# Kernel optimization log

Measured on AMD Instinct MI355X. Metric: run time of the kernel, lower is better.

Reference implementation:

```python
import jax, jax.numpy as jnp
import numpy as np

B, F, S, D = 256, 8, 200, 64
H = 36  # hidden units per field
EPS = 1e-3  # Dice BN epsilon


def setup_inputs() -> dict:
    key0 = jax.random.key(0)
    ks = jax.random.split(key0, 8)
    query = jax.random.normal(ks[0], (B, F, D), dtype=jnp.float32)
    key = jax.random.normal(ks[1], (B, F, S, D), dtype=jnp.float32)
    sequence_num = jax.random.randint(ks[2], (B, F), 1, S + 1, dtype=jnp.int32)
    W_h = jax.random.normal(ks[3], (F, 3 * D, H), dtype=jnp.float32) * 0.05
    b_h = jnp.zeros((F, H), dtype=jnp.float32)
    alpha = jnp.zeros((F,), dtype=jnp.float32)
    W_o = jax.random.normal(ks[4], (F, H, 1), dtype=jnp.float32) * 0.05
    b_o = jnp.zeros((F, 1), dtype=jnp.float32)
    return {"query": query, "key": key, "W_h": W_h, "b_h": b_h,
            "alpha": alpha, "W_o": W_o, "b_o": b_o,
            "sequence_num": sequence_num, "training": 1}


def reference(query, key, W_h, b_h, alpha, W_o, b_o, sequence_num, training):
    # query: [B,F,D], key: [B,F,S,D]
    q = query[:, :, None, :]                      # broadcast instead of tile
    qb = jnp.broadcast_to(q, key.shape)           # [B,F,S,D]
    cat = jnp.concatenate([key, qb, q - key], axis=-1)  # [B,F,S,3D]
    # per-field Dense(36), vectorized across fields
    h = jnp.einsum('bfsc,fch->bfsh', cat, W_h) + b_h[None, :, None, :]
    # Dice: BatchNorm (no affine, training-mode batch stats over batch+seq per field/feature)
    mean = h.mean(axis=(0, 2), keepdims=True)
    var = h.var(axis=(0, 2), keepdims=True)
    p = jax.nn.sigmoid((h - mean) * jax.lax.rsqrt(var + EPS))
    h = (alpha[None, :, None, None] * (1.0 - p) + p) * h
    # per-field Dense(1) -> attention scores [B,F,S]
    scores = jnp.einsum('bfsh,fh->bfs', h, W_o[:, :, 0]) + b_o[None, :, 0, None]
    # mask invalid positions and softmax over sequence
    mask = jnp.arange(key.shape[2])[None, None, :] < sequence_num[:, :, None]
    scores = jnp.where(mask, scores, -jnp.inf)
    attn = jax.nn.softmax(scores, axis=-1)        # [B,F,S]
    # weighted sum over sequence -> [B,F,D]
    return jnp.einsum('bfs,bfsd->bfd', attn, key)
```

## Files before the change

kernel.cpp:

```cpp
#include <hip/hip_runtime.h>
#include <math.h>

#define NB 256
#define NF 8
#define NS 200
#define ND 64
#define NH 36
#define MT 13
#define EPSV 1e-3f

#define WS_SUM 0
#define WS_SQ  288
#define WS_QT  1152
#define WS_WK  (1152 + 2048 * 48)

typedef __attribute__((ext_vector_type(8))) short short8;
typedef __attribute__((ext_vector_type(4))) float f32x4;

__device__ __forceinline__ unsigned short f32_to_bf16(float x) {
    unsigned u = __float_as_uint(x);
    unsigned r = u + 0x7FFFu + ((u >> 16) & 1u);
    return (unsigned short)(r >> 16);
}
__device__ __forceinline__ float bf16_to_f32(unsigned short h) {
    return __uint_as_float(((unsigned)h) << 16);
}
__device__ __forceinline__ short8 cvt8(float4 a, float4 b) {
    short8 r;
    r[0] = (short)f32_to_bf16(a.x); r[1] = (short)f32_to_bf16(a.y);
    r[2] = (short)f32_to_bf16(a.z); r[3] = (short)f32_to_bf16(a.w);
    r[4] = (short)f32_to_bf16(b.x); r[5] = (short)f32_to_bf16(b.y);
    r[6] = (short)f32_to_bf16(b.z); r[7] = (short)f32_to_bf16(b.w);
    return r;
}

__global__ __launch_bounds__(256) void k_prep(
    const float* __restrict__ query, const float* __restrict__ W_h,
    const float* __restrict__ b_h, float* __restrict__ ws)
{
    const int blk = blockIdx.x, tid = threadIdx.x;
    if (blk < NB) {
        __shared__ float qs[NF * ND];
        for (int i = tid; i < NF * ND; i += 256)
            qs[i] = query[(size_t)blk * NF * ND + i];
        __syncthreads();
        for (int i = tid; i < NF * 48; i += 256) {
            int f = i / 48, h = i - f * 48;
            float acc = 0.f;
            if (h < NH) {
                const float* Wf = W_h + (size_t)f * (3 * ND * NH);
                acc = b_h[f * NH + h];
                for (int d = 0; d < ND; ++d)
                    acc += qs[f * ND + d] * (Wf[(ND + d) * NH + h] + Wf[(2 * ND + d) * NH + h]);
            }
            ws[WS_QT + (size_t)(blk * NF + f) * 48 + h] = acc;
        }
    } else {
        const int f = blk - NB;
        const float* Wf = W_h + (size_t)f * (3 * ND * NH);
        unsigned short* wk = (unsigned short*)(ws + WS_WK) + f * (48 * ND);
        for (int i = tid; i < 48 * ND; i += 256) {
            int h = i >> 6, d = i & 63;
            float v = (h < NH) ? (Wf[d * NH + h] - Wf[(2 * ND + d) * NH + h]) : 0.f;
            wk[h * ND + d] = f32_to_bf16(v);
        }
    }
}

__global__ __launch_bounds__(256, 4) void k_stats(
    const float* __restrict__ key, float* __restrict__ ws)
{
    const int blk = blockIdx.x;
    const int f = blk & (NF - 1);
    const int tid = threadIdx.x;
    const int lane = tid & 63;
    const int wv = tid >> 6;
    const int col = lane & 15;
    const int quad = lane >> 4;

    __shared__ float sumP[48], sqP[48];
    if (tid < 48) { sumP[tid] = 0.f; sqP[tid] = 0.f; }
    __syncthreads();

    const float* kbase = key + (size_t)blk * (NS * ND);
    const unsigned short* wk = (const unsigned short*)(ws + WS_WK) + f * (48 * ND);

    short8 bfr[3][2];
    float qv[3];
    #pragma unroll
    for (int nt = 0; nt < 3; ++nt) {
        #pragma unroll
        for (int ks = 0; ks < 2; ++ks)
            bfr[nt][ks] = *(const short8*)&wk[(nt * 16 + col) * ND + ks * 32 + quad * 8];
        qv[nt] = ws[WS_QT + (size_t)blk * 48 + nt * 16 + col];
    }

    float s_sum[3] = {0.f, 0.f, 0.f}, s_sq[3] = {0.f, 0.f, 0.f};
    for (int mt = wv; mt < MT; mt += 4) {
        const int s = 16 * mt + col;
        const float4* p = (const float4*)(kbase + (size_t)(s < NS ? s : NS - 1) * ND + quad * 8);
        float4 a0 = p[0], a1 = p[1];
        float4 b0 = p[8], b1 = p[9];
        short8 ah0 = cvt8(a0, a1);
        short8 ah1 = cvt8(b0, b1);
        #pragma unroll
        for (int nt = 0; nt < 3; ++nt) {
            f32x4 acc = {qv[nt], qv[nt], qv[nt], qv[nt]};
            acc = __builtin_amdgcn_mfma_f32_16x16x32_bf16(ah0, bfr[nt][0], acc, 0, 0, 0);
            acc = __builtin_amdgcn_mfma_f32_16x16x32_bf16(ah1, bfr[nt][1], acc, 0, 0, 0);
            #pragma unroll
            for (int r = 0; r < 4; ++r) {
                int srow = 16 * mt + quad * 4 + r;
                if (srow < NS) { float v = acc[r]; s_sum[nt] += v; s_sq[nt] += v * v; }
            }
        }
    }
    #pragma unroll
    for (int nt = 0; nt < 3; ++nt) {
        float sv = s_sum[nt], qq = s_sq[nt];
        sv += __shfl_xor(sv, 16, 64); sv += __shfl_xor(sv, 32, 64);
        qq += __shfl_xor(qq, 16, 64); qq += __shfl_xor(qq, 32, 64);
        if (quad == 0) {
            atomicAdd(&sumP[nt * 16 + col], sv);
            atomicAdd(&sqP[nt * 16 + col], qq);
        }
    }
    __syncthreads();
    if (tid < NH) {
        atomicAdd(&ws[WS_SUM + f * NH + tid], sumP[tid]);
        atomicAdd(&ws[WS_SQ + f * NH + tid], sqP[tid]);
    }
}

__global__ __launch_bounds__(256, 3) void k_attn(
    const float* __restrict__ key, const float* __restrict__ alpha,
    const float* __restrict__ W_o, const float* __restrict__ b_o,
    const int* __restrict__ seqn, const float* __restrict__ ws,
    float* __restrict__ out)
{
    const int blk = blockIdx.x;
    const int f = blk & (NF - 1);
    const int tid = threadIdx.x;
    const int lane = tid & 63;
    const int wv = tid >> 6;
    const int col = lane & 15;
    const int quad = lane >> 4;

    __shared__ float sw[208];
    __shared__ float redM[4], redS[4];
    __shared__ float pout[4][64];

    const float* kbase = key + (size_t)blk * (NS * ND);
    const unsigned short* wk = (const unsigned short*)(ws + WS_WK) + f * (48 * ND);
    const float inv_n = 1.f / (float)(NB * NS);

    short8 bfr[3][2];
    float qv[3], mn[3], iv[3], wo[3];
    #pragma unroll
    for (int nt = 0; nt < 3; ++nt) {
        #pragma unroll
        for (int ks = 0; ks < 2; ++ks)
            bfr[nt][ks] = *(const short8*)&wk[(nt * 16 + col) * ND + ks * 32 + quad * 8];
        const int hh = nt * 16 + col;
        const bool hv = hh < NH;
        const int hc = hv ? hh : 0;
        qv[nt] = ws[WS_QT + (size_t)blk * 48 + hh];
        const float sm = ws[WS_SUM + f * NH + hc];
        const float sq = ws[WS_SQ + f * NH + hc];
        const float m = sm * inv_n;
        mn[nt] = m;
        iv[nt] = rsqrtf(fmaxf(sq * inv_n - m * m, 0.f) + EPSV);
        wo[nt] = hv ? W_o[f * NH + hh] : 0.f;
    }
    const float alf = alpha[f];
    const float bo = b_o[f];
    const int sq_n = seqn[blk];

    short8 kah[4][2];
    #pragma unroll
    for (int t = 0; t < 4; ++t) {
        const int mt = wv + 4 * t;
        if (mt < MT) {
            const int s = 16 * mt + col;
            const float4* p = (const float4*)(kbase + (size_t)(s < NS ? s : NS - 1) * ND + quad * 8);
            float4 a0 = p[0], a1 = p[1];
            float4 b0 = p[8], b1 = p[9];
            kah[t][0] = cvt8(a0, a1);
            kah[t][1] = cvt8(b0, b1);
            float part[4] = {0.f, 0.f, 0.f, 0.f};
            #pragma unroll
            for (int nt = 0; nt < 3; ++nt) {
                f32x4 acc = {qv[nt], qv[nt], qv[nt], qv[nt]};
                acc = __builtin_amdgcn_mfma_f32_16x16x32_bf16(kah[t][0], bfr[nt][0], acc, 0, 0, 0);
                acc = __builtin_amdgcn_mfma_f32_16x16x32_bf16(kah[t][1], bfr[nt][1], acc, 0, 0, 0);
                #pragma unroll
                for (int r = 0; r < 4; ++r) {
                    const float h = acc[r];
                    const float pg = 1.f / (1.f + __expf(-(h - mn[nt]) * iv[nt]));
                    part[r] += (alf + (1.f - alf) * pg) * h * wo[nt];
                }
            }
            #pragma unroll
            for (int r = 0; r < 4; ++r) {
                float v = part[r];
                v += __shfl_xor(v, 1, 64);
                v += __shfl_xor(v, 2, 64);
                v += __shfl_xor(v, 4, 64);
                v += __shfl_xor(v, 8, 64);
                const int srow = 16 * mt + quad * 4 + r;
                if (col == 0 && srow < NS) sw[srow] = v + bo;
            }
        }
    }
    __syncthreads();

    const bool valid = (tid < 208) && (tid < sq_n);
    const float sc = valid ? sw[tid] : -1e30f;
    float m = sc;
    m = fmaxf(m, __shfl_xor(m, 1, 64));  m = fmaxf(m, __shfl_xor(m, 2, 64));
    m = fmaxf(m, __shfl_xor(m, 4, 64));  m = fmaxf(m, __shfl_xor(m, 8, 64));
    m = fmaxf(m, __shfl_xor(m, 16, 64)); m = fmaxf(m, __shfl_xor(m, 32, 64));
    if (lane == 0) redM[wv] = m;
    __syncthreads();
    const float maxv = fmaxf(fmaxf(redM[0], redM[1]), fmaxf(redM[2], redM[3]));
    const float e = valid ? __expf(sc - maxv) : 0.f;
    float l = e;
    l += __shfl_xor(l, 1, 64);  l += __shfl_xor(l, 2, 64);
    l += __shfl_xor(l, 4, 64);  l += __shfl_xor(l, 8, 64);
    l += __shfl_xor(l, 16, 64); l += __shfl_xor(l, 32, 64);
    if (lane == 0) redS[wv] = l;
    __syncthreads();
    const float isum = 1.f / (redS[0] + redS[1] + redS[2] + redS[3]);
    if (tid < 208) sw[tid] = e * isum;
    __syncthreads();

    float po0[8] = {0,0,0,0,0,0,0,0}, po1[8] = {0,0,0,0,0,0,0,0};
    #pragma unroll
    for (int t = 0; t < 4; ++t) {
        const int mt = wv + 4 * t;
        if (mt < MT) {
            const float w = sw[16 * mt + col];
            #pragma unroll
            for (int j = 0; j < 8; ++j) {
                po0[j] += w * bf16_to_f32((unsigned short)kah[t][0][j]);
                po1[j] += w * bf16_to_f32((unsigned short)kah[t][1][j]);
            }
        }
    }
    #pragma unroll
    for (int off = 1; off <= 8; off <<= 1) {
        #pragma unroll
        for (int j = 0; j < 8; ++j) {
            po0[j] += __shfl_xor(po0[j], off, 64);
            po1[j] += __shfl_xor(po1[j], off, 64);
        }
    }
    if (col == 0) {
        #pragma unroll
        for (int j = 0; j < 8; ++j) {
            pout[wv][quad * 8 + j] = po0[j];
            pout[wv][32 + quad * 8 + j] = po1[j];
        }
    }
    __syncthreads();
    if (tid < 64)
        out[(size_t)blk * ND + tid] =
            pout[0][tid] + pout[1][tid] + pout[2][tid] + pout[3][tid];
}

extern "C" void kernel_launch(void* const* d_in, const int* in_sizes, int n_in,
                              void* d_out, int out_size, void* d_ws, size_t ws_size,
                              hipStream_t stream) {
    const float* query = (const float*)d_in[0];
    const float* key   = (const float*)d_in[1];
    const float* W_h   = (const float*)d_in[2];
    const float* b_h   = (const float*)d_in[3];
    const float* alpha = (const float*)d_in[4];
    const float* W_o   = (const float*)d_in[5];
    const float* b_o   = (const float*)d_in[6];
    const int*   seqn  = (const int*)d_in[7];
    float* out = (float*)d_out;
    float* ws  = (float*)d_ws;

    hipMemsetAsync(ws, 0, 576 * sizeof(float), stream);
    k_prep<<<NB + NF, 256, 0, stream>>>(query, W_h, b_h, ws);
    k_stats<<<NB * NF, 256, 0, stream>>>(key, ws);
    k_attn<<<NB * NF, 256, 0, stream>>>(key, alpha, W_o, b_o, seqn, ws, out);
}
```

Measured before the change: 213.1 us.

## Process two batch rows per block, fold query term into stats algebraically

Each stats and attention block now handles two (batch, field) pairs, so half as many blocks are launched. The stats kernel no longer adds the per-row query term inside the MFMA. It adds that term afterwards in closed form, using the sums and squared sums of the key projection. The 200-row tail is peeled into a separate partial tile so the per-row bound checks go away, and the attention kernel's occupancy hint rises from 3 to 4. Float-to-bf16 conversion now truncates with a byte permute instead of rounding to nearest even, which is cheaper but slightly less accurate.

```diff
diff --git a/kernel.cpp b/kernel.cpp
--- a/kernel.cpp
+++ b/kernel.cpp
@@ -6,7 +6,6 @@
 #define NS 200
 #define ND 64
 #define NH 36
-#define MT 13
 #define EPSV 1e-3f
 
 #define WS_SUM 0
@@ -16,8 +15,9 @@
 
 typedef __attribute__((ext_vector_type(8))) short short8;
 typedef __attribute__((ext_vector_type(4))) float f32x4;
-
-__device__ __forceinline__ unsigned short f32_to_bf16(float x) {
+typedef __attribute__((ext_vector_type(4))) int int4v;
+
+__device__ __forceinline__ unsigned short f32_to_bf16_rne(float x) {
     unsigned u = __float_as_uint(x);
     unsigned r = u + 0x7FFFu + ((u >> 16) & 1u);
     return (unsigned short)(r >> 16);
@@ -25,13 +25,13 @@
 __device__ __forceinline__ float bf16_to_f32(unsigned short h) {
     return __uint_as_float(((unsigned)h) << 16);
 }
-__device__ __forceinline__ short8 cvt8(float4 a, float4 b) {
-    short8 r;
-    r[0] = (short)f32_to_bf16(a.x); r[1] = (short)f32_to_bf16(a.y);
-    r[2] = (short)f32_to_bf16(a.z); r[3] = (short)f32_to_bf16(a.w);
-    r[4] = (short)f32_to_bf16(b.x); r[5] = (short)f32_to_bf16(b.y);
-    r[6] = (short)f32_to_bf16(b.z); r[7] = (short)f32_to_bf16(b.w);
-    return r;
+__device__ __forceinline__ short8 pack8(float4 a, float4 b) {
+    int4v t;
+    t[0] = (int)__builtin_amdgcn_perm(__float_as_uint(a.y), __float_as_uint(a.x), 0x07060302u);
+    t[1] = (int)__builtin_amdgcn_perm(__float_as_uint(a.w), __float_as_uint(a.z), 0x07060302u);
+    t[2] = (int)__builtin_amdgcn_perm(__float_as_uint(b.y), __float_as_uint(b.x), 0x07060302u);
+    t[3] = (int)__builtin_amdgcn_perm(__float_as_uint(b.w), __float_as_uint(b.z), 0x07060302u);
+    return __builtin_bit_cast(short8, t);
 }
 
 __global__ __launch_bounds__(256) void k_prep(
@@ -62,7 +62,7 @@
         for (int i = tid; i < 48 * ND; i += 256) {
             int h = i >> 6, d = i & 63;
             float v = (h < NH) ? (Wf[d * NH + h] - Wf[(2 * ND + d) * NH + h]) : 0.f;
-            wk[h * ND + d] = f32_to_bf16(v);
+            wk[h * ND + d] = f32_to_bf16_rne(v);
         }
     }
 }
@@ -72,67 +72,95 @@
 {
     const int blk = blockIdx.x;
     const int f = blk & (NF - 1);
+    const int b0 = (blk >> 3) * 2;
     const int tid = threadIdx.x;
     const int lane = tid & 63;
     const int wv = tid >> 6;
     const int col = lane & 15;
     const int quad = lane >> 4;
 
-    __shared__ float sumP[48], sqP[48];
-    if (tid < 48) { sumP[tid] = 0.f; sqP[tid] = 0.f; }
+    __shared__ float sumP[2][48], sqP[2][48];
+    if (tid < 96) { int p = tid / 48, h = tid - 48 * p; sumP[p][h] = 0.f; sqP[p][h] = 0.f; }
     __syncthreads();
 
-    const float* kbase = key + (size_t)blk * (NS * ND);
     const unsigned short* wk = (const unsigned short*)(ws + WS_WK) + f * (48 * ND);
+    const float* kb0 = key + (size_t)(b0 * NF + f) * (NS * ND);
+    const float* kb1 = kb0 + (size_t)NF * NS * ND;
 
     short8 bfr[3][2];
-    float qv[3];
     #pragma unroll
-    for (int nt = 0; nt < 3; ++nt) {
+    for (int nt = 0; nt < 3; ++nt)
         #pragma unroll
         for (int ks = 0; ks < 2; ++ks)
             bfr[nt][ks] = *(const short8*)&wk[(nt * 16 + col) * ND + ks * 32 + quad * 8];
-        qv[nt] = ws[WS_QT + (size_t)blk * 48 + nt * 16 + col];
-    }
-
-    float s_sum[3] = {0.f, 0.f, 0.f}, s_sq[3] = {0.f, 0.f, 0.f};
-    for (int mt = wv; mt < MT; mt += 4) {
-        const int s = 16 * mt + col;
-        const float4* p = (const float4*)(kbase + (size_t)(s < NS ? s : NS - 1) * ND + quad * 8);
-        float4 a0 = p[0], a1 = p[1];
-        float4 b0 = p[8], b1 = p[9];
-        short8 ah0 = cvt8(a0, a1);
-        short8 ah1 = cvt8(b0, b1);
+
+    float s1[2][3] = {{0.f,0.f,0.f},{0.f,0.f,0.f}};
+    float s2[2][3] = {{0.f,0.f,0.f},{0.f,0.f,0.f}};
+
+    #pragma unroll
+    for (int i = 0; i < 3; ++i) {
+        const int s = 16 * (wv + 4 * i) + col;
+        const size_t off = (size_t)s * ND + quad * 8;
+        #pragma unroll
+        for (int p = 0; p < 2; ++p) {
+            const float4* ptr = (const float4*)((p ? kb1 : kb0) + off);
+            float4 a0 = ptr[0], a1 = ptr[1], c0 = ptr[8], c1 = ptr[9];
+            short8 fa = pack8(a0, a1);
+            short8 fb = pack8(c0, c1);
+            #pragma unroll
+            for (int nt = 0; nt < 3; ++nt) {
+                f32x4 acc = {0.f, 0.f, 0.f, 0.f};
+                acc = __builtin_amdgcn_mfma_f32_16x16x32_bf16(fa, bfr[nt][0], acc, 0, 0, 0);
+                acc = __builtin_amdgcn_mfma_f32_16x16x32_bf16(fb, bfr[nt][1], acc, 0, 0, 0);
+                #pragma unroll
+                for (int r = 0; r < 4; ++r) { float v = acc[r]; s1[p][nt] += v; s2[p][nt] += v * v; }
+            }
+        }
+    }
+    if (wv == 0) {
+        const int s = 192 + col;
+        #pragma unroll
+        for (int p = 0; p < 2; ++p) {
+            short8 fa = {0,0,0,0,0,0,0,0}, fb = {0,0,0,0,0,0,0,0};
+            if (col < 8) {
+                const float4* ptr = (const float4*)((p ? kb1 : kb0) + (size_t)s * ND + quad * 8);
+                float4 a0 = ptr[0], a1 = ptr[1], c0 = ptr[8], c1 = ptr[9];
+                fa = pack8(a0, a1); fb = pack8(c0, c1);
+            }
+            #pragma unroll
+            for (int nt = 0; nt < 3; ++nt) {
+                f32x4 acc = {0.f, 0.f, 0.f, 0.f};
+                acc = __builtin_amdgcn_mfma_f32_16x16x32_bf16(fa, bfr[nt][0], acc, 0, 0, 0);
+                acc = __builtin_amdgcn_mfma_f32_16x16x32_bf16(fb, bfr[nt][1], acc, 0, 0, 0);
+                #pragma unroll
+                for (int r = 0; r < 4; ++r) { float v = acc[r]; s1[p][nt] += v; s2[p][nt] += v * v; }
+            }
+        }
+    }
+    #pragma unroll
+    for (int p = 0; p < 2; ++p)
         #pragma unroll
         for (int nt = 0; nt < 3; ++nt) {
-            f32x4 acc = {qv[nt], qv[nt], qv[nt], qv[nt]};
-            acc = __builtin_amdgcn_mfma_f32_16x16x32_bf16(ah0, bfr[nt][0], acc, 0, 0, 0);
-            acc = __builtin_amdgcn_mfma_f32_16x16x32_bf16(ah1, bfr[nt][1], acc, 0, 0, 0);
-            #pragma unroll
-            for (int r = 0; r < 4; ++r) {
-                int srow = 16 * mt + quad * 4 + r;
-                if (srow < NS) { float v = acc[r]; s_sum[nt] += v; s_sq[nt] += v * v; }
-            }
-        }
-    }
-    #pragma unroll
-    for (int nt = 0; nt < 3; ++nt) {
-        float sv = s_sum[nt], qq = s_sq[nt];
-        sv += __shfl_xor(sv, 16, 64); sv += __shfl_xor(sv, 32, 64);
-        qq += __shfl_xor(qq, 16, 64); qq += __shfl_xor(qq, 32, 64);
-        if (quad == 0) {
-            atomicAdd(&sumP[nt * 16 + col], sv);
-            atomicAdd(&sqP[nt * 16 + col], qq);
-        }
-    }
+            float a = s1[p][nt], c = s2[p][nt];
+            a += __shfl_xor(a, 16, 64); a += __shfl_xor(a, 32, 64);
+            c += __shfl_xor(c, 16, 64); c += __shfl_xor(c, 32, 64);
+            if (quad == 0) {
+                atomicAdd(&sumP[p][nt * 16 + col], a);
+                atomicAdd(&sqP[p][nt * 16 + col], c);
+            }
+        }
     __syncthreads();
-    if (tid < NH) {
-        atomicAdd(&ws[WS_SUM + f * NH + tid], sumP[tid]);
-        atomicAdd(&ws[WS_SQ + f * NH + tid], sqP[tid]);
-    }
-}
-
-__global__ __launch_bounds__(256, 3) void k_attn(
+    if (tid < 72) {
+        const int p = (tid >= NH) ? 1 : 0;
+        const int h = tid - NH * p;
+        const float S1 = sumP[p][h], S2 = sqP[p][h];
+        const float qt = ws[WS_QT + (size_t)((b0 + p) * NF + f) * 48 + h];
+        atomicAdd(&ws[WS_SUM + f * NH + h], S1 + 200.f * qt);
+        atomicAdd(&ws[WS_SQ  + f * NH + h], S2 + 2.f * qt * S1 + 200.f * qt * qt);
+    }
+}
+
+__global__ __launch_bounds__(256, 4) void k_attn(
     const float* __restrict__ key, const float* __restrict__ alpha,
     const float* __restrict__ W_o, const float* __restrict__ b_o,
     const int* __restrict__ seqn, const float* __restrict__ ws,
@@ -140,6 +168,7 @@
 {
     const int blk = blockIdx.x;
     const int f = blk & (NF - 1);
+    const int b0 = (blk >> 3) * 2;
     const int tid = threadIdx.x;
     const int lane = tid & 63;
     const int wv = tid >> 6;
@@ -150,12 +179,11 @@
     __shared__ float redM[4], redS[4];
     __shared__ float pout[4][64];
 
-    const float* kbase = key + (size_t)blk * (NS * ND);
     const unsigned short* wk = (const unsigned short*)(ws + WS_WK) + f * (48 * ND);
     const float inv_n = 1.f / (float)(NB * NS);
 
     short8 bfr[3][2];
-    float qv[3], mn[3], iv[3], wo[3];
+    float mn[3], iv[3], wo[3];
     #pragma unroll
     for (int nt = 0; nt < 3; ++nt) {
         #pragma unroll
@@ -164,7 +192,6 @@
         const int hh = nt * 16 + col;
         const bool hv = hh < NH;
         const int hc = hv ? hh : 0;
-        qv[nt] = ws[WS_QT + (size_t)blk * 48 + hh];
         const float sm = ws[WS_SUM + f * NH + hc];
         const float sq = ws[WS_SQ + f * NH + hc];
         const float m = sm * inv_n;
@@ -174,25 +201,31 @@
     }
     const float alf = alpha[f];
     const float bo = b_o[f];
-    const int sq_n = seqn[blk];
-
-    short8 kah[4][2];
-    #pragma unroll
-    for (int t = 0; t < 4; ++t) {
-        const int mt = wv + 4 * t;
-        if (mt < MT) {
+
+    for (int p = 0; p < 2; ++p) {
+        const int bf = (b0 + p) * NF + f;
+        const float* kbase = key + (size_t)bf * (NS * ND);
+        float qv[3];
+        #pragma unroll
+        for (int nt = 0; nt < 3; ++nt)
+            qv[nt] = ws[WS_QT + (size_t)bf * 48 + nt * 16 + col];
+        const int sq_n = seqn[bf];
+
+        short8 kah[4][2];
+        #pragma unroll
+        for (int i = 0; i < 3; ++i) {
+            const int mt = wv + 4 * i;
             const int s = 16 * mt + col;
-            const float4* p = (const float4*)(kbase + (size_t)(s < NS ? s : NS - 1) * ND + quad * 8);
-            float4 a0 = p[0], a1 = p[1];
-            float4 b0 = p[8], b1 = p[9];
-            kah[t][0] = cvt8(a0, a1);
-            kah[t][1] = cvt8(b0, b1);
+            const float4* ptr = (const float4*)(kbase + (size_t)s * ND + quad * 8);
+            float4 a0 = ptr[0], a1 = ptr[1], c0 = ptr[8], c1 = ptr[9];
+            kah[i][0] = pack8(a0, a1);
+            kah[i][1] = pack8(c0, c1);
             float part[4] = {0.f, 0.f, 0.f, 0.f};
             #pragma unroll
             for (int nt = 0; nt < 3; ++nt) {
                 f32x4 acc = {qv[nt], qv[nt], qv[nt], qv[nt]};
-                acc = __builtin_amdgcn_mfma_f32_16x16x32_bf16(kah[t][0], bfr[nt][0], acc, 0, 0, 0);
-                acc = __builtin_amdgcn_mfma_f32_16x16x32_bf16(kah[t][1], bfr[nt][1], acc, 0, 0, 0);
+                acc = __builtin_amdgcn_mfma_f32_16x16x32_bf16(kah[i][0], bfr[nt][0], acc, 0, 0, 0);
+                acc = __builtin_amdgcn_mfma_f32_16x16x32_bf16(kah[i][1], bfr[nt][1], acc, 0, 0, 0);
                 #pragma unroll
                 for (int r = 0; r < 4; ++r) {
                     const float h = acc[r];
@@ -203,69 +236,102 @@
             #pragma unroll
             for (int r = 0; r < 4; ++r) {
                 float v = part[r];
-                v += __shfl_xor(v, 1, 64);
-                v += __shfl_xor(v, 2, 64);
-                v += __shfl_xor(v, 4, 64);
-                v += __shfl_xor(v, 8, 64);
-                const int srow = 16 * mt + quad * 4 + r;
+                v += __shfl_xor(v, 1, 64); v += __shfl_xor(v, 2, 64);
+                v += __shfl_xor(v, 4, 64); v += __shfl_xor(v, 8, 64);
+                if (col == 0) sw[16 * mt + quad * 4 + r] = v + bo;
+            }
+        }
+        if (wv == 0) {
+            kah[3][0] = (short8){0,0,0,0,0,0,0,0};
+            kah[3][1] = (short8){0,0,0,0,0,0,0,0};
+            if (col < 8) {
+                const float4* ptr = (const float4*)(kbase + (size_t)(192 + col) * ND + quad * 8);
+                float4 a0 = ptr[0], a1 = ptr[1], c0 = ptr[8], c1 = ptr[9];
+                kah[3][0] = pack8(a0, a1);
+                kah[3][1] = pack8(c0, c1);
+            }
+            float part[4] = {0.f, 0.f, 0.f, 0.f};
+            #pragma unroll
+            for (int nt = 0; nt < 3; ++nt) {
+                f32x4 acc = {qv[nt], qv[nt], qv[nt], qv[nt]};
+                acc = __builtin_amdgcn_mfma_f32_16x16x32_bf16(kah[3][0], bfr[nt][0], acc, 0, 0, 0);
+                acc = __builtin_amdgcn_mfma_f32_16x16x32_bf16(kah[3][1], bfr[nt][1], acc, 0, 0, 0);
+                #pragma unroll
+                for (int r = 0; r < 4; ++r) {
+                    const float h = acc[r];
+                    const float pg = 1.f / (1.f + __expf(-(h - mn[nt]) * iv[nt]));
+                    part[r] += (alf + (1.f - alf) * pg) * h * wo[nt];
+                }
+            }
+            #pragma unroll
+            for (int r = 0; r < 4; ++r) {
+                float v = part[r];
+                v += __shfl_xor(v, 1, 64); v += __shfl_xor(v, 2, 64);
+                v += __shfl_xor(v, 4, 64); v += __shfl_xor(v, 8, 64);
+                const int srow = 192 + quad * 4 + r;
                 if (col == 0 && srow < NS) sw[srow] = v + bo;
             }
         }
-    }
-    __syncthreads();
-
-    const bool valid = (tid < 208) && (tid < sq_n);
-    const float sc = valid ? sw[tid] : -1e30f;
-    float m = sc;
-    m = fmaxf(m, __shfl_xor(m, 1, 64));  m = fmaxf(m, __shfl_xor(m, 2, 64));
-    m = fmaxf(m, __shfl_xor(m, 4, 64));  m = fmaxf(m, __shfl_xor(m, 8, 64));
-    m = fmaxf(m, __shfl_xor(m, 16, 64)); m = fmaxf(m, __shfl_xor(m, 32, 64));
-    if (lane == 0) redM[wv] = m;
-    __syncthreads();
-    const float maxv = fmaxf(fmaxf(redM[0], redM[1]), fmaxf(redM[2], redM[3]));
-    const float e = valid ? __expf(sc - maxv) : 0.f;
-    float l = e;
-    l += __shfl_xor(l, 1, 64);  l += __shfl_xor(l, 2, 64);
-    l += __shfl_xor(l, 4, 64);  l += __shfl_xor(l, 8, 64);
-    l += __shfl_xor(l, 16, 64); l += __shfl_xor(l, 32, 64);
-    if (lane == 0) redS[wv] = l;
-    __syncthreads();
-    const float isum = 1.f / (redS[0] + redS[1] + redS[2] + redS[3]);
-    if (tid < 208) sw[tid] = e * isum;
-    __syncthreads();
-
-    float po0[8] = {0,0,0,0,0,0,0,0}, po1[8] = {0,0,0,0,0,0,0,0};
-    #pragma unroll
-    for (int t = 0; t < 4; ++t) {
-        const int mt = wv + 4 * t;
-        if (mt < MT) {
-            const float w = sw[16 * mt + col];
+        __syncthreads();
+
+        const bool valid = (tid < NS) && (tid < sq_n);
+        const float sc = valid ? sw[tid] : -1e30f;
+        float m = sc;
+        m = fmaxf(m, __shfl_xor(m, 1, 64));  m = fmaxf(m, __shfl_xor(m, 2, 64));
+        m = fmaxf(m, __shfl_xor(m, 4, 64));  m = fmaxf(m, __shfl_xor(m, 8, 64));
+        m = fmaxf(m, __shfl_xor(m, 16, 64)); m = fmaxf(m, __shfl_xor(m, 32, 64));
+        if (lane == 0) redM[wv] = m;
+        __syncthreads();
+        const float maxv = fmaxf(fmaxf(redM[0], redM[1]), fmaxf(redM[2], redM[3]));
+        const float e = valid ? __expf(sc - maxv) : 0.f;
+        float l = e;
+        l += __shfl_xor(l, 1, 64);  l += __shfl_xor(l, 2, 64);
+        l += __shfl_xor(l, 4, 64);  l += __shfl_xor(l, 8, 64);
+        l += __shfl_xor(l, 16, 64); l += __shfl_xor(l, 32, 64);
+        if (lane == 0) redS[wv] = l;
+        __syncthreads();
+        const float isum = 1.f / (redS[0] + redS[1] + redS[2] + redS[3]);
+        if (tid < 208) sw[tid] = e * isum;
+        __syncthreads();
+
+        float po0[8] = {0,0,0,0,0,0,0,0}, po1[8] = {0,0,0,0,0,0,0,0};
+        #pragma unroll
+        for (int i = 0; i < 3; ++i) {
+            const float w = sw[16 * (wv + 4 * i) + col];
             #pragma unroll
             for (int j = 0; j < 8; ++j) {
-                po0[j] += w * bf16_to_f32((unsigned short)kah[t][0][j]);
-                po1[j] += w * bf16_to_f32((unsigned short)kah[t][1][j]);
-            }
-        }
-    }
-    #pragma unroll
-    for (int off = 1; off <= 8; off <<= 1) {
-        #pragma unroll
-        for (int j = 0; j < 8; ++j) {
-            po0[j] += __shfl_xor(po0[j], off, 64);
-            po1[j] += __shfl_xor(po1[j], off, 64);
-        }
-    }
-    if (col == 0) {
-        #pragma unroll
-        for (int j = 0; j < 8; ++j) {
-            pout[wv][quad * 8 + j] = po0[j];
-            pout[wv][32 + quad * 8 + j] = po1[j];
-        }
-    }
-    __syncthreads();
-    if (tid < 64)
-        out[(size_t)blk * ND + tid] =
-            pout[0][tid] + pout[1][tid] + pout[2][tid] + pout[3][tid];
+                po0[j] += w * bf16_to_f32((unsigned short)kah[i][0][j]);
+                po1[j] += w * bf16_to_f32((unsigned short)kah[i][1][j]);
+            }
+        }
+        if (wv == 0) {
+            const float w = sw[192 + col];
+            #pragma unroll
+            for (int j = 0; j < 8; ++j) {
+                po0[j] += w * bf16_to_f32((unsigned short)kah[3][0][j]);
+                po1[j] += w * bf16_to_f32((unsigned short)kah[3][1][j]);
+            }
+        }
+        #pragma unroll
+        for (int off = 1; off <= 8; off <<= 1) {
+            #pragma unroll
+            for (int j = 0; j < 8; ++j) {
+                po0[j] += __shfl_xor(po0[j], off, 64);
+                po1[j] += __shfl_xor(po1[j], off, 64);
+            }
+        }
+        if (col == 0) {
+            #pragma unroll
+            for (int j = 0; j < 8; ++j) {
+                pout[wv][quad * 8 + j] = po0[j];
+                pout[wv][32 + quad * 8 + j] = po1[j];
+            }
+        }
+        __syncthreads();
+        if (tid < 64)
+            out[(size_t)bf * ND + tid] =
+                pout[0][tid] + pout[1][tid] + pout[2][tid] + pout[3][tid];
+    }
 }
 
 extern "C" void kernel_launch(void* const* d_in, const int* in_sizes, int n_in,
@@ -284,6 +350,6 @@
 
     hipMemsetAsync(ws, 0, 576 * sizeof(float), stream);
     k_prep<<<NB + NF, 256, 0, stream>>>(query, W_h, b_h, ws);
-    k_stats<<<NB * NF, 256, 0, stream>>>(key, ws);
-    k_attn<<<NB * NF, 256, 0, stream>>>(key, alpha, W_o, b_o, seqn, ws, out);
-}
+    k_stats<<<NB * NF / 2, 256, 0, stream>>>(key, ws);
+    k_attn<<<NB * NF / 2, 256, 0, stream>>>(key, alpha, W_o, b_o, seqn, ws, out);
+}
```

After: 216.1 us. Within noise of the previous version (+1.4%).

## Fuse prep, stats and attention into one persistent kernel with grid barrier

Applied to the files above, without the earlier changes.

Replaces the three kernels with a single 256-block, 512-thread kernel. Each block handles 8 batch rows of one field, computes the query projection and bf16 weights in LDS, accumulates BN statistics, waits at a global atomic grid barrier, then computes attention per row. It also converts to bf16 by truncation with v_perm instead of round-to-nearest, and double-buffers key loads in the stats pass. The aim is to cut launch overhead and the separate prep pass. The cost is that key is reread after the barrier, only 256 blocks run, and the barrier depends on all blocks being co-resident.

```diff
diff --git a/kernel.cpp b/kernel.cpp
--- a/kernel.cpp
+++ b/kernel.cpp
@@ -6,18 +6,18 @@
 #define NS 200
 #define ND 64
 #define NH 36
-#define MT 13
 #define EPSV 1e-3f
+#define GRID_BLKS 256
 
 #define WS_SUM 0
 #define WS_SQ  288
-#define WS_QT  1152
-#define WS_WK  (1152 + 2048 * 48)
+#define WS_BAR 576
 
 typedef __attribute__((ext_vector_type(8))) short short8;
 typedef __attribute__((ext_vector_type(4))) float f32x4;
-
-__device__ __forceinline__ unsigned short f32_to_bf16(float x) {
+typedef __attribute__((ext_vector_type(4))) int int4v;
+
+__device__ __forceinline__ unsigned short f32_to_bf16_rne(float x) {
     unsigned u = __float_as_uint(x);
     unsigned r = u + 0x7FFFu + ((u >> 16) & 1u);
     return (unsigned short)(r >> 16);
@@ -25,148 +25,156 @@
 __device__ __forceinline__ float bf16_to_f32(unsigned short h) {
     return __uint_as_float(((unsigned)h) << 16);
 }
-__device__ __forceinline__ short8 cvt8(float4 a, float4 b) {
-    short8 r;
-    r[0] = (short)f32_to_bf16(a.x); r[1] = (short)f32_to_bf16(a.y);
-    r[2] = (short)f32_to_bf16(a.z); r[3] = (short)f32_to_bf16(a.w);
-    r[4] = (short)f32_to_bf16(b.x); r[5] = (short)f32_to_bf16(b.y);
-    r[6] = (short)f32_to_bf16(b.z); r[7] = (short)f32_to_bf16(b.w);
-    return r;
-}
-
-__global__ __launch_bounds__(256) void k_prep(
-    const float* __restrict__ query, const float* __restrict__ W_h,
-    const float* __restrict__ b_h, float* __restrict__ ws)
-{
-    const int blk = blockIdx.x, tid = threadIdx.x;
-    if (blk < NB) {
-        __shared__ float qs[NF * ND];
-        for (int i = tid; i < NF * ND; i += 256)
-            qs[i] = query[(size_t)blk * NF * ND + i];
-        __syncthreads();
-        for (int i = tid; i < NF * 48; i += 256) {
-            int f = i / 48, h = i - f * 48;
-            float acc = 0.f;
-            if (h < NH) {
-                const float* Wf = W_h + (size_t)f * (3 * ND * NH);
-                acc = b_h[f * NH + h];
-                for (int d = 0; d < ND; ++d)
-                    acc += qs[f * ND + d] * (Wf[(ND + d) * NH + h] + Wf[(2 * ND + d) * NH + h]);
-            }
-            ws[WS_QT + (size_t)(blk * NF + f) * 48 + h] = acc;
-        }
-    } else {
-        const int f = blk - NB;
-        const float* Wf = W_h + (size_t)f * (3 * ND * NH);
-        unsigned short* wk = (unsigned short*)(ws + WS_WK) + f * (48 * ND);
-        for (int i = tid; i < 48 * ND; i += 256) {
-            int h = i >> 6, d = i & 63;
-            float v = (h < NH) ? (Wf[d * NH + h] - Wf[(2 * ND + d) * NH + h]) : 0.f;
-            wk[h * ND + d] = f32_to_bf16(v);
-        }
-    }
-}
-
-__global__ __launch_bounds__(256, 4) void k_stats(
-    const float* __restrict__ key, float* __restrict__ ws)
+__device__ __forceinline__ short8 pack8(float4 a, float4 b) {
+    int4v t;
+    t[0] = (int)__builtin_amdgcn_perm(__float_as_uint(a.y), __float_as_uint(a.x), 0x07060302u);
+    t[1] = (int)__builtin_amdgcn_perm(__float_as_uint(a.w), __float_as_uint(a.z), 0x07060302u);
+    t[2] = (int)__builtin_amdgcn_perm(__float_as_uint(b.y), __float_as_uint(b.x), 0x07060302u);
+    t[3] = (int)__builtin_amdgcn_perm(__float_as_uint(b.w), __float_as_uint(b.z), 0x07060302u);
+    return __builtin_bit_cast(short8, t);
+}
+
+__global__ __launch_bounds__(512, 2) void k_fused(
+    const float* __restrict__ query, const float* __restrict__ key,
+    const float* __restrict__ W_h, const float* __restrict__ b_h,
+    const float* __restrict__ alpha, const float* __restrict__ W_o,
+    const float* __restrict__ b_o, const int* __restrict__ seqn,
+    float* __restrict__ ws, float* __restrict__ out)
 {
     const int blk = blockIdx.x;
     const int f = blk & (NF - 1);
+    const int b0 = (blk >> 3) * 8;
     const int tid = threadIdx.x;
     const int lane = tid & 63;
     const int wv = tid >> 6;
     const int col = lane & 15;
     const int quad = lane >> 4;
 
+    __shared__ __align__(16) unsigned short wkL[48 * 72];
+    __shared__ float qs[8][64];
+    __shared__ float qts[8][48];
     __shared__ float sumP[48], sqP[48];
+    __shared__ float sw[208];
+    __shared__ float redM[8], redS[8];
+    __shared__ float pout[8][64];
+
+    const float* Wf = W_h + (size_t)f * (3 * ND * NH);
+    const size_t bstride = (size_t)NF * NS * ND;
+    const float* kb0 = key + (size_t)(b0 * NF + f) * (NS * ND);
+
+    {
+        int p = tid >> 6, d = tid & 63;
+        qs[p][d] = query[(size_t)((b0 + p) * NF + f) * ND + d];
+    }
+    for (int i = tid; i < 48 * 64; i += 512) {
+        int h = i >> 6, d = i & 63;
+        float v = (h < NH) ? (Wf[d * NH + h] - Wf[(2 * ND + d) * NH + h]) : 0.f;
+        wkL[h * 72 + d] = f32_to_bf16_rne(v);
+    }
     if (tid < 48) { sumP[tid] = 0.f; sqP[tid] = 0.f; }
     __syncthreads();
 
-    const float* kbase = key + (size_t)blk * (NS * ND);
-    const unsigned short* wk = (const unsigned short*)(ws + WS_WK) + f * (48 * ND);
-
+    if (tid < 384) {
+        const int p = tid / 48, hh = tid % 48;
+        float acc = 0.f;
+        if (hh < NH) {
+            acc = b_h[f * NH + hh];
+            #pragma unroll 8
+            for (int d = 0; d < ND; ++d)
+                acc += qs[p][d] * (Wf[(ND + d) * NH + hh] + Wf[(2 * ND + d) * NH + hh]);
+        }
+        qts[p][hh] = acc;
+    }
     short8 bfr[3][2];
-    float qv[3];
+    #pragma unroll
+    for (int nt = 0; nt < 3; ++nt)
+        #pragma unroll
+        for (int ks = 0; ks < 2; ++ks)
+            bfr[nt][ks] = *(const short8*)&wkL[(nt * 16 + col) * 72 + ks * 32 + quad * 8];
+    __syncthreads();
+
+    float s1[3] = {0.f, 0.f, 0.f}, s2[3] = {0.f, 0.f, 0.f};
+    float4 Lb[2][2][4];
+
+    auto load_tiles = [&](int j, float4 L[2][4]) {
+        const float* kb = kb0 + (size_t)j * bstride;
+        #pragma unroll
+        for (int i = 0; i < 2; ++i) {
+            const int mt = wv + 8 * i;
+            if (mt <= 12) {
+                const int s = 16 * mt + col;
+                const float4* ptr = (const float4*)(kb + (size_t)(s < NS ? s : NS - 1) * ND + quad * 8);
+                L[i][0] = ptr[0]; L[i][1] = ptr[1]; L[i][2] = ptr[8]; L[i][3] = ptr[9];
+            }
+        }
+    };
+
+    load_tiles(0, Lb[0]);
+    for (int j = 0; j < 8; ++j) {
+        if (j < 7) load_tiles(j + 1, Lb[(j + 1) & 1]);
+        float4 (*L)[4] = Lb[j & 1];
+        const float qv0 = qts[j][col], qv1 = qts[j][16 + col], qv2 = qts[j][32 + col];
+        const float qv[3] = {qv0, qv1, qv2};
+        #pragma unroll
+        for (int i = 0; i < 2; ++i) {
+            const int mt = wv + 8 * i;
+            if (mt <= 12) {
+                short8 fa = pack8(L[i][0], L[i][1]);
+                short8 fb = pack8(L[i][2], L[i][3]);
+                #pragma unroll
+                for (int nt = 0; nt < 3; ++nt) {
+                    f32x4 acc = {qv[nt], qv[nt], qv[nt], qv[nt]};
+                    acc = __builtin_amdgcn_mfma_f32_16x16x32_bf16(fa, bfr[nt][0], acc, 0, 0, 0);
+                    acc = __builtin_amdgcn_mfma_f32_16x16x32_bf16(fb, bfr[nt][1], acc, 0, 0, 0);
+                    if (mt < 12) {
+                        #pragma unroll
+                        for (int r = 0; r < 4; ++r) { float v = acc[r]; s1[nt] += v; s2[nt] += v * v; }
+                    } else {
+                        const int base_s = 192 + quad * 4;
+                        #pragma unroll
+                        for (int r = 0; r < 4; ++r)
+                            if (base_s + r < NS) { float v = acc[r]; s1[nt] += v; s2[nt] += v * v; }
+                    }
+                }
+            }
+        }
+    }
+
     #pragma unroll
     for (int nt = 0; nt < 3; ++nt) {
-        #pragma unroll
-        for (int ks = 0; ks < 2; ++ks)
-            bfr[nt][ks] = *(const short8*)&wk[(nt * 16 + col) * ND + ks * 32 + quad * 8];
-        qv[nt] = ws[WS_QT + (size_t)blk * 48 + nt * 16 + col];
-    }
-
-    float s_sum[3] = {0.f, 0.f, 0.f}, s_sq[3] = {0.f, 0.f, 0.f};
-    for (int mt = wv; mt < MT; mt += 4) {
-        const int s = 16 * mt + col;
-        const float4* p = (const float4*)(kbase + (size_t)(s < NS ? s : NS - 1) * ND + quad * 8);
-        float4 a0 = p[0], a1 = p[1];
-        float4 b0 = p[8], b1 = p[9];
-        short8 ah0 = cvt8(a0, a1);
-        short8 ah1 = cvt8(b0, b1);
-        #pragma unroll
-        for (int nt = 0; nt < 3; ++nt) {
-            f32x4 acc = {qv[nt], qv[nt], qv[nt], qv[nt]};
-            acc = __builtin_amdgcn_mfma_f32_16x16x32_bf16(ah0, bfr[nt][0], acc, 0, 0, 0);
-            acc = __builtin_amdgcn_mfma_f32_16x16x32_bf16(ah1, bfr[nt][1], acc, 0, 0, 0);
-            #pragma unroll
-            for (int r = 0; r < 4; ++r) {
-                int srow = 16 * mt + quad * 4 + r;
-                if (srow < NS) { float v = acc[r]; s_sum[nt] += v; s_sq[nt] += v * v; }
-            }
-        }
-    }
+        float a = s1[nt], c = s2[nt];
+        a += __shfl_xor(a, 16, 64); a += __shfl_xor(a, 32, 64);
+        c += __shfl_xor(c, 16, 64); c += __shfl_xor(c, 32, 64);
+        if (quad == 0) {
+            atomicAdd(&sumP[nt * 16 + col], a);
+            atomicAdd(&sqP[nt * 16 + col], c);
+        }
+    }
+    __syncthreads();
+    if (tid < NH) {
+        atomicAdd(&ws[WS_SUM + f * NH + tid], sumP[tid]);
+        atomicAdd(&ws[WS_SQ  + f * NH + tid], sqP[tid]);
+    }
+    __syncthreads();
+
+    if (tid == 0) {
+        __threadfence();
+        unsigned* cnt = (unsigned*)(ws + WS_BAR);
+        __hip_atomic_fetch_add(cnt, 1u, __ATOMIC_ACQ_REL, __HIP_MEMORY_SCOPE_AGENT);
+        while (__hip_atomic_load(cnt, __ATOMIC_ACQUIRE, __HIP_MEMORY_SCOPE_AGENT) < (unsigned)GRID_BLKS)
+            __builtin_amdgcn_s_sleep(8);
+    }
+    __syncthreads();
+
+    const float inv_n = 1.f / (float)(NB * NS);
+    float mn[3], iv[3], wo[3];
     #pragma unroll
     for (int nt = 0; nt < 3; ++nt) {
-        float sv = s_sum[nt], qq = s_sq[nt];
-        sv += __shfl_xor(sv, 16, 64); sv += __shfl_xor(sv, 32, 64);
-        qq += __shfl_xor(qq, 16, 64); qq += __shfl_xor(qq, 32, 64);
-        if (quad == 0) {
-            atomicAdd(&sumP[nt * 16 + col], sv);
-            atomicAdd(&sqP[nt * 16 + col], qq);
-        }
-    }
-    __syncthreads();
-    if (tid < NH) {
-        atomicAdd(&ws[WS_SUM + f * NH + tid], sumP[tid]);
-        atomicAdd(&ws[WS_SQ + f * NH + tid], sqP[tid]);
-    }
-}
-
-__global__ __launch_bounds__(256, 3) void k_attn(
-    const float* __restrict__ key, const float* __restrict__ alpha,
-    const float* __restrict__ W_o, const float* __restrict__ b_o,
-    const int* __restrict__ seqn, const float* __restrict__ ws,
-    float* __restrict__ out)
-{
-    const int blk = blockIdx.x;
-    const int f = blk & (NF - 1);
-    const int tid = threadIdx.x;
-    const int lane = tid & 63;
-    const int wv = tid >> 6;
-    const int col = lane & 15;
-    const int quad = lane >> 4;
-
-    __shared__ float sw[208];
-    __shared__ float redM[4], redS[4];
-    __shared__ float pout[4][64];
-
-    const float* kbase = key + (size_t)blk * (NS * ND);
-    const unsigned short* wk = (const unsigned short*)(ws + WS_WK) + f * (48 * ND);
-    const float inv_n = 1.f / (float)(NB * NS);
-
-    short8 bfr[3][2];
-    float qv[3], mn[3], iv[3], wo[3];
-    #pragma unroll
-    for (int nt = 0; nt < 3; ++nt) {
-        #pragma unroll
-        for (int ks = 0; ks < 2; ++ks)
-            bfr[nt][ks] = *(const short8*)&wk[(nt * 16 + col) * ND + ks * 32 + quad * 8];
         const int hh = nt * 16 + col;
         const bool hv = hh < NH;
         const int hc = hv ? hh : 0;
-        qv[nt] = ws[WS_QT + (size_t)blk * 48 + hh];
-        const float sm = ws[WS_SUM + f * NH + hc];
-        const float sq = ws[WS_SQ + f * NH + hc];
+        const float sm = __hip_atomic_load(&ws[WS_SUM + f * NH + hc], __ATOMIC_RELAXED, __HIP_MEMORY_SCOPE_AGENT);
+        const float sq = __hip_atomic_load(&ws[WS_SQ  + f * NH + hc], __ATOMIC_RELAXED, __HIP_MEMORY_SCOPE_AGENT);
         const float m = sm * inv_n;
         mn[nt] = m;
         iv[nt] = rsqrtf(fmaxf(sq * inv_n - m * m, 0.f) + EPSV);
@@ -174,98 +182,110 @@
     }
     const float alf = alpha[f];
     const float bo = b_o[f];
-    const int sq_n = seqn[blk];
-
-    short8 kah[4][2];
-    #pragma unroll
-    for (int t = 0; t < 4; ++t) {
-        const int mt = wv + 4 * t;
-        if (mt < MT) {
-            const int s = 16 * mt + col;
-            const float4* p = (const float4*)(kbase + (size_t)(s < NS ? s : NS - 1) * ND + quad * 8);
-            float4 a0 = p[0], a1 = p[1];
-            float4 b0 = p[8], b1 = p[9];
-            kah[t][0] = cvt8(a0, a1);
-            kah[t][1] = cvt8(b0, b1);
-            float part[4] = {0.f, 0.f, 0.f, 0.f};
-            #pragma unroll
-            for (int nt = 0; nt < 3; ++nt) {
-                f32x4 acc = {qv[nt], qv[nt], qv[nt], qv[nt]};
-                acc = __builtin_amdgcn_mfma_f32_16x16x32_bf16(kah[t][0], bfr[nt][0], acc, 0, 0, 0);
-                acc = __builtin_amdgcn_mfma_f32_16x16x32_bf16(kah[t][1], bfr[nt][1], acc, 0, 0, 0);
+
+    for (int j = 0; j < 8; ++j) {
+        const int bfi = (b0 + j) * NF + f;
+        const float* kb = kb0 + (size_t)j * bstride;
+        const int sq_n = seqn[bfi];
+        const float qv[3] = {qts[j][col], qts[j][16 + col], qts[j][32 + col]};
+
+        short8 kah[2][2];
+        #pragma unroll
+        for (int i = 0; i < 2; ++i) {
+            const int mt = wv + 8 * i;
+            if (mt <= 12) {
+                const int s = 16 * mt + col;
+                const float4* ptr = (const float4*)(kb + (size_t)(s < NS ? s : NS - 1) * ND + quad * 8);
+                float4 a0 = ptr[0], a1 = ptr[1], c0 = ptr[8], c1 = ptr[9];
+                kah[i][0] = pack8(a0, a1);
+                kah[i][1] = pack8(c0, c1);
+                float part[4] = {0.f, 0.f, 0.f, 0.f};
+                #pragma unroll
+                for (int nt = 0; nt < 3; ++nt) {
+                    f32x4 acc = {qv[nt], qv[nt], qv[nt], qv[nt]};
+                    acc = __builtin_amdgcn_mfma_f32_16x16x32_bf16(kah[i][0], bfr[nt][0], acc, 0, 0, 0);
+                    acc = __builtin_amdgcn_mfma_f32_16x16x32_bf16(kah[i][1], bfr[nt][1], acc, 0, 0, 0);
+                    #pragma unroll
+                    for (int r = 0; r < 4; ++r) {
+                        const float h = acc[r];
+                        const float pg = 1.f / (1.f + __expf(-(h - mn[nt]) * iv[nt]));
+                        part[r] += (alf + (1.f - alf) * pg) * h * wo[nt];
+                    }
+                }
                 #pragma unroll
                 for (int r = 0; r < 4; ++r) {
-                    const float h = acc[r];
-                    const float pg = 1.f / (1.f + __expf(-(h - mn[nt]) * iv[nt]));
-                    part[r] += (alf + (1.f - alf) * pg) * h * wo[nt];
+                    float v = part[r];
+                    v += __shfl_xor(v, 1, 64); v += __shfl_xor(v, 2, 64);
+                    v += __shfl_xor(v, 4, 64); v += __shfl_xor(v, 8, 64);
+                    const int srow = 16 * mt + quad * 4 + r;
+                    if (col == 0 && srow < NS) sw[srow] = v + bo;
                 }
             }
+        }
+        __syncthreads();
+
+        const bool valid = (tid < NS) && (tid < sq_n);
+        const float sc = valid ? sw[tid] : -1e30f;
+        float m = sc;
+        m = fmaxf(m, __shfl_xor(m, 1, 64));  m = fmaxf(m, __shfl_xor(m, 2, 64));
+        m = fmaxf(m, __shfl_xor(m, 4, 64));  m = fmaxf(m, __shfl_xor(m, 8, 64));
+        m = fmaxf(m, __shfl_xor(m, 16, 64)); m = fmaxf(m, __shfl_xor(m, 32, 64));
+        if (lane == 0) redM[wv] = m;
+        __syncthreads();
+        float maxv = redM[0];
+        #pragma unroll
+        for (int w = 1; w < 8; ++w) maxv = fmaxf(maxv, redM[w]);
+        const float e = valid ? __expf(sc - maxv) : 0.f;
+        float l = e;
+        l += __shfl_xor(l, 1, 64);  l += __shfl_xor(l, 2, 64);
+        l += __shfl_xor(l, 4, 64);  l += __shfl_xor(l, 8, 64);
+        l += __shfl_xor(l, 16, 64); l += __shfl_xor(l, 32, 64);
+        if (lane == 0) redS[wv] = l;
+        __syncthreads();
+        float tot = redS[0];
+        #pragma unroll
+        for (int w = 1; w < 8; ++w) tot += redS[w];
+        const float isum = 1.f / tot;
+        if (tid < 208) sw[tid] = e * isum;
+        __syncthreads();
+
+        float po0[8] = {0,0,0,0,0,0,0,0}, po1[8] = {0,0,0,0,0,0,0,0};
+        #pragma unroll
+        for (int i = 0; i < 2; ++i) {
+            const int mt = wv + 8 * i;
+            if (mt <= 12) {
+                const float w = sw[16 * mt + col];
+                #pragma unroll
+                for (int jj = 0; jj < 8; ++jj) {
+                    po0[jj] += w * bf16_to_f32((unsigned short)kah[i][0][jj]);
+                    po1[jj] += w * bf16_to_f32((unsigned short)kah[i][1][jj]);
+                }
+            }
+        }
+        #pragma unroll
+        for (int off = 1; off <= 8; off <<= 1) {
             #pragma unroll
-            for (int r = 0; r < 4; ++r) {
-                float v = part[r];
-                v += __shfl_xor(v, 1, 64);
-                v += __shfl_xor(v, 2, 64);
-                v += __shfl_xor(v, 4, 64);
-                v += __shfl_xor(v, 8, 64);
-                const int srow = 16 * mt + quad * 4 + r;
-                if (col == 0 && srow < NS) sw[srow] = v + bo;
-            }
-        }
-    }
-    __syncthreads();
-
-    const bool valid = (tid < 208) && (tid < sq_n);
-    const float sc = valid ? sw[tid] : -1e30f;
-    float m = sc;
-    m = fmaxf(m, __shfl_xor(m, 1, 64));  m = fmaxf(m, __shfl_xor(m, 2, 64));
-    m = fmaxf(m, __shfl_xor(m, 4, 64));  m = fmaxf(m, __shfl_xor(m, 8, 64));
-    m = fmaxf(m, __shfl_xor(m, 16, 64)); m = fmaxf(m, __shfl_xor(m, 32, 64));
-    if (lane == 0) redM[wv] = m;
-    __syncthreads();
-    const float maxv = fmaxf(fmaxf(redM[0], redM[1]), fmaxf(redM[2], redM[3]));
-    const float e = valid ? __expf(sc - maxv) : 0.f;
-    float l = e;
-    l += __shfl_xor(l, 1, 64);  l += __shfl_xor(l, 2, 64);
-    l += __shfl_xor(l, 4, 64);  l += __shfl_xor(l, 8, 64);
-    l += __shfl_xor(l, 16, 64); l += __shfl_xor(l, 32, 64);
-    if (lane == 0) redS[wv] = l;
-    __syncthreads();
-    const float isum = 1.f / (redS[0] + redS[1] + redS[2] + redS[3]);
-    if (tid < 208) sw[tid] = e * isum;
-    __syncthreads();
-
-    float po0[8] = {0,0,0,0,0,0,0,0}, po1[8] = {0,0,0,0,0,0,0,0};
-    #pragma unroll
-    for (int t = 0; t < 4; ++t) {
-        const int mt = wv + 4 * t;
-        if (mt < MT) {
-            const float w = sw[16 * mt + col];
+            for (int jj = 0; jj < 8; ++jj) {
+                po0[jj] += __shfl_xor(po0[jj], off, 64);
+                po1[jj] += __shfl_xor(po1[jj], off, 64);
+            }
+        }
+        if (col == 0) {
             #pragma unroll
-            for (int j = 0; j < 8; ++j) {
-                po0[j] += w * bf16_to_f32((unsigned short)kah[t][0][j]);
-                po1[j] += w * bf16_to_f32((unsigned short)kah[t][1][j]);
-            }
-        }
-    }
-    #pragma unroll
-    for (int off = 1; off <= 8; off <<= 1) {
-        #pragma unroll
-        for (int j = 0; j < 8; ++j) {
-            po0[j] += __shfl_xor(po0[j], off, 64);
-            po1[j] += __shfl_xor(po1[j], off, 64);
-        }
-    }
-    if (col == 0) {
-        #pragma unroll
-        for (int j = 0; j < 8; ++j) {
-            pout[wv][quad * 8 + j] = po0[j];
-            pout[wv][32 + quad * 8 + j] = po1[j];
-        }
-    }
-    __syncthreads();
-    if (tid < 64)
-        out[(size_t)blk * ND + tid] =
-            pout[0][tid] + pout[1][tid] + pout[2][tid] + pout[3][tid];
+            for (int jj = 0; jj < 8; ++jj) {
+                pout[wv][quad * 8 + jj] = po0[jj];
+                pout[wv][32 + quad * 8 + jj] = po1[jj];
+            }
+        }
+        __syncthreads();
+        if (tid < 64) {
+            float o = 0.f;
+            #pragma unroll
+            for (int w = 0; w < 8; ++w) o += pout[w][tid];
+            out[(size_t)bfi * ND + tid] = o;
+        }
+        __syncthreads();
+    }
 }
 
 extern "C" void kernel_launch(void* const* d_in, const int* in_sizes, int n_in,
@@ -282,8 +302,6 @@
     float* out = (float*)d_out;
     float* ws  = (float*)d_ws;
 
-    hipMemsetAsync(ws, 0, 576 * sizeof(float), stream);
-    k_prep<<<NB + NF, 256, 0, stream>>>(query, W_h, b_h, ws);
-    k_stats<<<NB * NF, 256, 0, stream>>>(key, ws);
-    k_attn<<<NB * NF, 256, 0, stream>>>(key, alpha, W_o, b_o, seqn, ws, out);
-}
+    hipMemsetAsync(ws, 0, 578 * sizeof(float), stream);
+    k_fused<<<GRID_BLKS, 512, 0, stream>>>(query, key, W_h, b_h, alpha, W_o, b_o, seqn, ws, out);
+}
```

Result: slower. 249.9 us (+17.3%).
